# Performance work log

Hardware: AMD Instinct MI355X
Metric: run time of the kernel (lower is better)

## Reference

```python
import jax, jax.numpy as jnp
import numpy as np

NL, NS, NE = 16, 256, 100   # nlatent, nspatial, n_embd
B, P, T = 2, 2, 12


def _xavier(key, shape):
    # torch xavier_uniform: fan_in = shape[1]*prod(rest), fan_out = shape[0]*prod(rest)
    rf = int(np.prod(shape[2:])) if len(shape) > 2 else 1
    fan_in, fan_out = shape[1] * rf, shape[0] * rf
    b = float(np.sqrt(6.0 / (fan_in + fan_out)))
    return jax.random.uniform(key, shape, jnp.float32, -b, b)


def setup_inputs() -> dict:
    key = jax.random.key(0)
    ks = jax.random.split(key, 8)
    x = jax.random.normal(ks[0], (B, P, T, NL, NS), jnp.float32)
    K = _xavier(ks[1], (NS, NS, NL))
    Q = _xavier(ks[2], (NS, NS, NL))
    V = _xavier(ks[3], (NS, NS, NL))
    Aoo = jnp.ones((NS, NS), jnp.float32)
    # Ann is initialized to zeros in the module; use nonzero values so the
    # clamped geometric recurrence over time is actually exercised.
    Ann = jax.random.uniform(ks[4], (NE,), jnp.float32, -0.9, 0.9)
    Aon = _xavier(ks[5], (NS, NS, NE))
    Ano = _xavier(ks[6], (NS, NS, NE))
    w = jnp.ones((NS,), jnp.float32) / NS
    return {"x": x, "K": K, "Q": Q, "V": V, "Aoo": Aoo,
            "Ann": Ann, "Aon": Aon, "Ano": Ano, "w": w}


def reference(x, K, Q, V, Aoo, Ann, Aon, Ano, w):
    # kvt[B,p,T,X,Y] = sum_{x,c} Q[Y,x,c] K[X,x,c] x[B,p,T,c,x]
    kvt = jnp.einsum('Yxc,Xxc,BpTcx->BpTXY', Q, K, x)
    Aon_c = jnp.clip(Aon, -1.0, 1.0)
    Ano_c = jnp.clip(Ano, -1.0, 1.0)

    # t = T-1 term (elementwise Aoo) and t = T-2 term
    h = Aoo[None, None, None] * kvt[:, :, -1:]
    h = h + jnp.einsum('xyn,XYn,BpTXY->BpTxy', Aon_c, Ano_c, kvt[:, :, -2:-1])

    nT = x.shape[2]
    # Ann sequence used in the loop: A_2 = Ann (raw), A_{j+1} = clip(A_j * Ann)
    def step(a, _):
        return jnp.clip(a * Ann, -1.0, 1.0), a
    _, A_seq = jax.lax.scan(step, Ann, None, length=nT - 2)  # [T-2, n], A_seq[j-2]=A_j

    # loop index j=2..T-1 touches time slice t = T-1-j, i.e. t = T-3 .. 0
    s = jnp.einsum('XYn,BpJXY->BpJn', Ano_c, kvt[:, :, :nT - 2])  # J = t in 0..T-3
    A_t = A_seq[::-1]                       # align A_j with time index t = T-1-j
    s2 = jnp.einsum('Jn,BpJn->Bpn', A_t, s)
    h = h + jnp.einsum('xyn,Bpn->Bpxy', Aon_c, s2)[:, :, None]  # [B,p,1,x,y]

    q = jnp.einsum('Xxc,Bpcx->BpcX', V, x[:, :, -1])
    y = jnp.einsum('x,BpcX,BpTXx->BpTc', w, q, h)  # [B,p,1,c]
    return y
```

## Files before the change

### kernel.cpp

```cpp
#include <hip/hip_runtime.h>
#include <hip/hip_fp16.h>


using f32x4 = __attribute__((ext_vector_type(4))) float;
using half8 = __attribute__((ext_vector_type(8))) _Float16;
using half4 = __attribute__((ext_vector_type(4))) _Float16;

#define KVT_STRIDE 3145728ull
#define KS 4

__device__ inline float clip1(float v) { return fminf(fmaxf(v, -1.f), 1.f); }

__device__ inline half8 mul8(uint4 a, uint4 b) {
    half8 x = __builtin_bit_cast(half8, a);
    half8 y = __builtin_bit_cast(half8, b);
    return x * y;
}

__device__ __forceinline__ void gl_lds16(const void* g, void* l) {
    __builtin_amdgcn_global_load_lds(
        (const __attribute__((address_space(1))) void*)g,
        (__attribute__((address_space(3))) void*)l, 16, 0, 0);
}

__global__ void prep_kernel(const float* __restrict__ K, const float* __restrict__ Q,
                            const float* __restrict__ xin,
                            __half* __restrict__ Kh, __half* __restrict__ Qh,
                            __half* __restrict__ u_t)
{
    int b = blockIdx.x, t = threadIdx.x;
    if (b < 512) {
        bool isK = (b < 256);
        int bb = isK ? b : b - 256;
        size_t base = (size_t)bb * 4096 + t * 16;
        const f32x4* src = (const f32x4*)((isK ? K : Q) + base);
        __half* dst = (isK ? Kh : Qh) + base;
        #pragma unroll
        for (int j = 0; j < 2; ++j) {
            f32x4 v0 = src[j * 2], v1 = src[j * 2 + 1];
            half8 h;
            h[0] = (_Float16)v0.x; h[1] = (_Float16)v0.y;
            h[2] = (_Float16)v0.z; h[3] = (_Float16)v0.w;
            h[4] = (_Float16)v1.x; h[5] = (_Float16)v1.y;
            h[6] = (_Float16)v1.z; h[7] = (_Float16)v1.w;
            *(half8*)(dst + j * 8) = h;
        }
    } else {
        int bt = b - 512;
        const float* src = xin + (size_t)bt * 4096;
        int xx = t;
        half8 lo, hi;
        #pragma unroll
        for (int c = 0; c < 8; ++c)  lo[c] = (_Float16)src[c * 256 + xx];
        #pragma unroll
        for (int c = 0; c < 8; ++c)  hi[c] = (_Float16)src[(c + 8) * 256 + xx];
        half8* dst = (half8*)(u_t + (size_t)bt * 4096 + xx * 16);
        dst[0] = lo; dst[1] = hi;
    }
}

__global__ __launch_bounds__(256, 4) void gemm_kvt(
    const __half* __restrict__ Kh, const __half* __restrict__ Qh,
    const __half* __restrict__ u_t, __half* __restrict__ kvtp)
{
    __shared__ __half As[2][128][32];
    __shared__ __half Bs[2][128][32];
    __shared__ __half u_s[1024];

    int bid = blockIdx.x;
    int work = (bid & 7) * 96 + (bid >> 3);
    int kc = work / 192;
    int rem = work - kc * 192;
    int tile = rem / 48;
    int bt = rem - tile * 48;
    int Xb = (tile >> 1) * 128, Yb = (tile & 1) * 128;
    int kbase = kc * 1024;

    int tid = threadIdx.x;
    if (tid < 128)
        *(uint4*)&u_s[tid * 8] = *(const uint4*)(u_t + (size_t)bt * 4096 + kbase + tid * 8);
    __syncthreads();

    int wave = tid >> 6, lane = tid & 63;

    int arow = tid >> 1;
    int apair = (tid & 1) * 2;
    const __half* gA = Kh + (size_t)(Xb + arow) * 4096 + kbase + apair * 8;
    int aswz = (arow >> 1) & 3;
    int asb0 = ((apair + 0) ^ aswz) << 4;
    int asb1 = ((apair + 1) ^ aswz) << 4;

    int srow = lane >> 2;
    int sk = ((lane & 3) ^ ((srow >> 1) & 3)) << 3;
    const __half* gB = Qh + (size_t)(Yb + wave * 16 + srow) * 4096 + kbase + sk;

    int wr = (wave >> 1) * 64, wc = (wave & 1) * 64;
    int lrow = lane & 15, kg = lane >> 4;
    int fb = (kg * 16) ^ (((lrow >> 1) & 3) << 4);

    f32x4 acc[4][4];
    f32x4 zero = {0.f, 0.f, 0.f, 0.f};
    #pragma unroll
    for (int m = 0; m < 4; ++m)
        #pragma unroll
        for (int n = 0; n < 4; ++n) acc[m][n] = zero;

    #define ISSUE_B(s, buf)                                                    \
        do {                                                                   \
            _Pragma("unroll")                                                  \
            for (int i_ = 0; i_ < 2; ++i_)                                     \
                gl_lds16(gB + (size_t)(i_ * 64) * 4096 + (s) * 32,             \
                         &Bs[buf][i_ * 64 + wave * 16][0]);                    \
        } while (0)

    #define WRITE_A(s, r0, r1, buf)                                            \
        do {                                                                   \
            uint4 uv0 = *(const uint4*)&u_s[(s) * 32 + apair * 8];             \
            uint4 uv1 = *(const uint4*)&u_s[(s) * 32 + apair * 8 + 8];         \
            *(half8*)((char*)&As[buf][arow][0] + asb0) = mul8(r0, uv0);        \
            *(half8*)((char*)&As[buf][arow][0] + asb1) = mul8(r1, uv1);        \
        } while (0)

    #define COMPUTE(cur)                                                       \
        do {                                                                   \
            half8 af[4], bf[4];                                                \
            _Pragma("unroll")                                                  \
            for (int m = 0; m < 4; ++m)                                        \
                af[m] = *(const half8*)((const char*)&As[cur][wr + m * 16 + lrow][0] + fb); \
            _Pragma("unroll")                                                  \
            for (int n = 0; n < 4; ++n)                                        \
                bf[n] = *(const half8*)((const char*)&Bs[cur][wc + n * 16 + lrow][0] + fb); \
            _Pragma("unroll")                                                  \
            for (int m = 0; m < 4; ++m)                                        \
                _Pragma("unroll")                                              \
                for (int n = 0; n < 4; ++n)                                    \
                    acc[m][n] = __builtin_amdgcn_mfma_f32_16x16x32_f16(af[m], bf[n], acc[m][n], 0, 0, 0); \
        } while (0)

    #define STEP(s, c0, c1, i0, i1, cur)                                       \
        do {                                                                   \
            if ((s) < 31) asm volatile("s_waitcnt vmcnt(4) lgkmcnt(0)" ::: "memory"); \
            else          asm volatile("s_waitcnt vmcnt(0) lgkmcnt(0)" ::: "memory"); \
            __builtin_amdgcn_s_barrier();                                      \
            __builtin_amdgcn_sched_barrier(0);                                 \
            COMPUTE(cur);                                                      \
            asm volatile("s_waitcnt lgkmcnt(0)" ::: "memory");                 \
            __builtin_amdgcn_s_barrier();                                      \
            __builtin_amdgcn_sched_barrier(0);                                 \
            if ((s) + 2 < 32) {                                                \
                const __half* a_ = gA + ((s) + 2) * 32;                        \
                i0 = *(const uint4*)a_;                                        \
                i1 = *(const uint4*)(a_ + 8);                                  \
                ISSUE_B((s) + 2, cur);                                         \
            }                                                                  \
            if ((s) + 1 < 32) WRITE_A((s) + 1, c0, c1, (cur) ^ 1);             \
        } while (0)

    uint4 aP0, aP1, aC0, aC1;
    aP0 = *(const uint4*)gA;
    aP1 = *(const uint4*)(gA + 8);
    ISSUE_B(0, 0);
    aC0 = *(const uint4*)(gA + 32);
    aC1 = *(const uint4*)(gA + 40);
    ISSUE_B(1, 1);
    WRITE_A(0, aP0, aP1, 0);

    #pragma unroll
    for (int s = 0; s < 32; s += 2) {
        STEP(s,     aC0, aC1, aP0, aP1, 0);
        STEP(s + 1, aP0, aP1, aC0, aC1, 1);
    }
    #undef STEP
    #undef COMPUTE
    #undef WRITE_A
    #undef ISSUE_B

    __half* outp = kvtp + (size_t)kc * KVT_STRIDE + (size_t)bt * 65536;
    int row0 = Xb + wr + kg * 4;
    int col0 = Yb + wc + lrow;
    #pragma unroll
    for (int m = 0; m < 4; ++m)
        #pragma unroll
        for (int n = 0; n < 4; ++n)
            #pragma unroll
            for (int rr = 0; rr < 4; ++rr)
                outp[(size_t)(row0 + m * 16 + rr) * 256 + col0 + n * 16] =
                    __float2half(acc[m][n][rr]);
}

__global__ __launch_bounds__(256) void mid_kernel(
    const float* __restrict__ Ano, const __half* __restrict__ kvtp,
    const float* __restrict__ V, const float* __restrict__ xin,
    const float* __restrict__ Aon, const float* __restrict__ wv,
    float* __restrict__ Sp, float* __restrict__ R, float* __restrict__ W2p)
{
    __shared__ __align__(16) char smem[49792];
    int b = blockIdx.x, tid = threadIdx.x;

    if (b < 256) {
        __half* anoA = (__half*)smem;
        __half* anoB = (__half*)(smem + 12928);
        float (*kvtA)[68] = (float(*)[68])(smem + 25856);
        float (*kvtB)[68] = (float(*)[68])(smem + 37824);
        int k0 = b * 256;

        int lane = tid & 63;
        int bp = tid >> 6;
        bool has2 = lane < 36;
        float acc0[11], acc1[11];
        #pragma unroll
        for (int J = 0; J < 11; ++J) { acc0[J] = 0.f; acc1[J] = 0.f; }

        f32x4 ar[7];
        half8 kr[2][4];

        #define LOAD_SP(cc)                                                    \
            do {                                                               \
                int k0s = k0 + (cc) * 64;                                      \
                const f32x4* asrc = (const f32x4*)(Ano + (size_t)k0s * 100);   \
                _Pragma("unroll")                                              \
                for (int it = 0; it < 7; ++it) {                               \
                    int i = tid + it * 256;                                    \
                    if (i < 1600) ar[it] = __builtin_nontemporal_load(asrc + i); \
                }                                                              \
                _Pragma("unroll")                                              \
                for (int it = 0; it < 2; ++it) {                               \
                    int idx = tid + it * 256;                                  \
                    if (idx < 352) {                                           \
                        int rI = idx >> 3, g = idx & 7;                        \
                        int bpr = rI / 11, Jr = rI - bpr * 11;                 \
                        const __half* p = kvtp + (size_t)(bpr * 12 + Jr) * 65536 + k0s + g * 8; \
                        kr[it][0] = *(const half8*)(p);                        \
                        kr[it][1] = *(const half8*)(p + KVT_STRIDE);           \
                        kr[it][2] = *(const half8*)(p + 2 * KVT_STRIDE);       \
                        kr[it][3] = *(const half8*)(p + 3 * KVT_STRIDE);       \
                    }                                                          \
                }                                                              \
            } while (0)

        #define WRITE_SP(anoDst, kvtDst)                                       \
            do {                                                               \
                _Pragma("unroll")                                              \
                for (int it = 0; it < 7; ++it) {                               \
                    int i = tid + it * 256;                                    \
                    if (i < 1600) {                                            \
                        half4 h;                                               \
                        h[0] = (_Float16)clip1(ar[it].x);                      \
                        h[1] = (_Float16)clip1(ar[it].y);                      \
                        h[2] = (_Float16)clip1(ar[it].z);                      \
                        h[3] = (_Float16)clip1(ar[it].w);                      \
                        *(half4*)&anoDst[i * 4] = h;                           \
                    }                                                          \
                }                                                              \
                _Pragma("unroll")                                              \
                for (int it = 0; it < 2; ++it) {                               \
                    int idx = tid + it * 256;                                  \
                    if (idx < 352) {                                           \
                        int rI = idx >> 3, g = idx & 7;                        \
                        f32x4 lo, hi;                                          \
                        _Pragma("unroll")                                      \
                        for (int j = 0; j < 4; ++j) {                          \
                            lo[j] = (float)kr[it][0][j] + (float)kr[it][1][j]  \
                                  + (float)kr[it][2][j] + (float)kr[it][3][j]; \
                            hi[j] = (float)kr[it][0][j+4] + (float)kr[it][1][j+4] \
                                  + (float)kr[it][2][j+4] + (float)kr[it][3][j+4]; \
                        }                                                      \
                        *(f32x4*)&kvtDst[rI][g * 8]     = lo;                  \
                        *(f32x4*)&kvtDst[rI][g * 8 + 4] = hi;                  \
                    }                                                          \
                }                                                              \
            } while (0)

        #define COMPUTE_SP(anoSrc, kvtSrc)                                     \
            do {                                                               \
                for (int k = 0; k < 64; k += 4) {                              \
                    f32x4 kv[11];                                              \
                    _Pragma("unroll")                                          \
                    for (int J = 0; J < 11; ++J)                               \
                        kv[J] = *(const f32x4*)&kvtSrc[bp * 11 + J][k];        \
                    _Pragma("unroll")                                          \
                    for (int kk = 0; kk < 4; ++kk) {                           \
                        float a0 = (float)anoSrc[(k + kk) * 100 + lane];       \
                        float a1r = (float)anoSrc[(k + kk) * 100 + 64 + lane]; \
                        float a1 = has2 ? a1r : 0.f;                           \
                        _Pragma("unroll")                                      \
                        for (int J = 0; J < 11; ++J) {                         \
                            acc0[J] += kv[J][kk] * a0;                         \
                            acc1[J] += kv[J][kk] * a1;                         \
                        }                                                      \
                    }                                                          \
                }                                                              \
            } while (0)

        LOAD_SP(0);
        WRITE_SP(anoA, kvtA);
        __syncthreads();
        LOAD_SP(1);
        COMPUTE_SP(anoA, kvtA);
        WRITE_SP(anoB, kvtB);
        __syncthreads();
        LOAD_SP(2);
        COMPUTE_SP(anoB, kvtB);
        WRITE_SP(anoA, kvtA);
        __syncthreads();
        LOAD_SP(3);
        COMPUTE_SP(anoA, kvtA);
        WRITE_SP(anoB, kvtB);
        __syncthreads();
        COMPUTE_SP(anoB, kvtB);

        #undef LOAD_SP
        #undef WRITE_SP
        #undef COMPUTE_SP

        float* outb = Sp + ((size_t)b * 4 + bp) * 1100;
        #pragma unroll
        for (int J = 0; J < 11; ++J) {
            outb[J * 100 + lane] = acc0[J];
            if (has2) outb[J * 100 + 64 + lane] = acc1[J];
        }
    } else if (b < 512) {
        float* vrow = (float*)smem;
        int X = b - 256;
        {
            const float4* src = (const float4*)(V + (size_t)X * 4096);
            float4* dst = (float4*)vrow;
            for (int i = tid; i < 1024; i += 256) dst[i] = src[i];
        }
        __syncthreads();
        int bp = tid >> 6, c = (tid >> 2) & 15, g = tid & 3;
        const float* xl = xin + ((size_t)(bp * 12) + 11) * 4096 + c * 256;
        float p = 0.f;
        #pragma unroll 4
        for (int x = g * 64; x < g * 64 + 64; ++x)
            p += xl[x] * vrow[x * 16 + c];
        p += __shfl_xor(p, 1);
        p += __shfl_xor(p, 2);
        if (g == 0) R[((size_t)bp * 256 + X) * 16 + c] = p;
    } else {
        int idx = b - 512;
        int X = idx >> 1, h = idx & 1;
        int g = h * 2 + (tid >> 7), n = tid & 127;
        if (n < 100) {
            const float* base = Aon + (size_t)X * 25600 + (size_t)g * 6400 + n;
            float acc = 0.f;
            for (int bb = 0; bb < 64; ++bb)
                acc += wv[g * 64 + bb] * clip1(__builtin_nontemporal_load(base + (size_t)bb * 100));
            W2p[((size_t)g * 256 + X) * 100 + n] = acc;
        }
    }
}

__global__ void reduce_s(const float* __restrict__ Sp, float* __restrict__ Sq,
                         float* __restrict__ out)
{
    int bid = blockIdx.x;
    int t = threadIdx.x;
    if (bid == 0 && t < 64) out[t] = 0.f;
    int qq = bid & 7, idx = bid >> 3;
    int bp = idx / 11, J = idx - bp * 11;
    if (t >= 100) return;
    float acc = 0.f;
    for (int c = qq * 32; c < qq * 32 + 32; ++c)
        acc += Sp[((size_t)c * 4 + bp) * 1100 + J * 100 + t];
    Sq[(size_t)(qq * 44 + idx) * 100 + t] = acc;
}

__global__ __launch_bounds__(256) void hw_kernel(const float* __restrict__ Aoo,
                                                 const float* __restrict__ wv,
                                                 const __half* __restrict__ kvtp,
                                                 const float* __restrict__ W2p,
                                                 const float* __restrict__ Sq,
                                                 const float* __restrict__ Ann,
                                                 const float* __restrict__ R,
                                                 float* __restrict__ out)
{
    __shared__ float yp[4][16];
    __shared__ float c2s[128];
    int bp = blockIdx.x >> 6, Xg = blockIdx.x & 63;
    int tid = threadIdx.x;

    if (tid < 128) {
        int n = tid;
        float r = 0.f;
        if (n < 100) {
            float S[11];
            #pragma unroll
            for (int J = 0; J < 11; ++J) {
                float s = 0.f;
                #pragma unroll
                for (int qq = 0; qq < 8; ++qq)
                    s += Sq[(size_t)(qq * 44 + bp * 11 + J) * 100 + n];
                S[J] = s;
            }
            float a = Ann[n];
            float seq[10];
            float v = a;
            seq[0] = v;
            #pragma unroll
            for (int s2 = 1; s2 < 10; ++s2) { v = clip1(v * a); seq[s2] = v; }
            r = S[10];
            #pragma unroll
            for (int J = 0; J < 10; ++J)
                r += seq[9 - J] * S[J];
        }
        c2s[n] = r;
    }
    __syncthreads();

    int wave = tid >> 6, lane = tid & 63;
    int X = Xg * 4 + wave;
    size_t base = (size_t)(bp * 12 + 11) * 65536 + (size_t)X * 256;
    const float* ao = Aoo + (size_t)X * 256;
    float red = 0.f;
    #pragma unroll
    for (int qq = 0; qq < 4; ++qq) {
        int xx = qq * 64 + lane;
        float kvv = 0.f;
        #pragma unroll
        for (int c = 0; c < KS; ++c)
            kvv += __half2float(kvtp[(size_t)c * KVT_STRIDE + base + xx]);
        red += wv[xx] * ao[xx] * kvv;
    }
    float w2a = 0.f, w2b = 0.f;
    #pragma unroll
    for (int g = 0; g < 4; ++g) {
        w2a += W2p[((size_t)g * 256 + X) * 100 + lane];
        if (lane < 36) w2b += W2p[((size_t)g * 256 + X) * 100 + 64 + lane];
    }
    red += c2s[lane] * w2a;
    if (lane < 36)
        red += c2s[64 + lane] * w2b;
    #pragma unroll
    for (int off = 32; off; off >>= 1) red += __shfl_xor(red, off);
    if (lane < 16) yp[wave][lane] = red * R[((size_t)bp * 256 + X) * 16 + lane];
    __syncthreads();
    if (tid < 16) {
        float s = yp[0][tid] + yp[1][tid] + yp[2][tid] + yp[3][tid];
        atomicAdd(&out[bp * 16 + tid], s);
    }
}

extern "C" void kernel_launch(void* const* d_in, const int* in_sizes, int n_in,
                              void* d_out, int out_size, void* d_ws, size_t ws_size,
                              hipStream_t stream)
{
    const float* x   = (const float*)d_in[0];
    const float* K   = (const float*)d_in[1];
    const float* Q   = (const float*)d_in[2];
    const float* V   = (const float*)d_in[3];
    const float* Aoo = (const float*)d_in[4];
    const float* Ann = (const float*)d_in[5];
    const float* Aon = (const float*)d_in[6];
    const float* Ano = (const float*)d_in[7];
    const float* wv  = (const float*)d_in[8];
    float* out = (float*)d_out;

    char* ws = (char*)d_ws;
    const size_t o_Qh   = 0;
    const size_t o_Kh   = o_Qh + (size_t)2 * 1024 * 1024;
    const size_t o_ut   = o_Kh + (size_t)2 * 1024 * 1024;
    const size_t o_kvtp = o_ut + (size_t)512 * 1024;
    const size_t o_Sp   = o_kvtp + (size_t)KS * KVT_STRIDE * 2;
    const size_t o_Sq   = o_Sp + (size_t)256 * 4400 * 4;
    const size_t o_W2   = o_Sq + (size_t)35200 * 4 + 64;
    const size_t o_R    = o_W2 + (size_t)102400 * 4;

    __half* Qh  = (__half*)(ws + o_Qh);
    __half* Kh  = (__half*)(ws + o_Kh);
    __half* u_t = (__half*)(ws + o_ut);
    __half* kvtp = (__half*)(ws + o_kvtp);
    float* Sp   = (float*)(ws + o_Sp);
    float* Sq   = (float*)(ws + o_Sq);
    float* W2p  = (float*)(ws + o_W2);
    float* R    = (float*)(ws + o_R);

    hipLaunchKernelGGL(prep_kernel, dim3(560),  dim3(256), 0, stream,
                       K, Q, x, Kh, Qh, u_t);
    hipLaunchKernelGGL(gemm_kvt,    dim3(768),  dim3(256), 0, stream,
                       Kh, Qh, u_t, kvtp);
    hipLaunchKernelGGL(mid_kernel,  dim3(1024), dim3(256), 0, stream,
                       Ano, kvtp, V, x, Aon, wv, Sp, R, W2p);
    hipLaunchKernelGGL(reduce_s,    dim3(352),  dim3(128), 0, stream, Sp, Sq, out);
    hipLaunchKernelGGL(hw_kernel,   dim3(256),  dim3(256), 0, stream,
                       Aoo, wv, kvtp, W2p, Sq, Ann, R, out);
}
```

Baseline: 88.95 us.

## Double K-tile depth in kvt GEMM and single-buffer the A tile

```diff
diff --git a/kernel.cpp b/kernel.cpp
--- a/kernel.cpp
+++ b/kernel.cpp
@@ -59,12 +59,12 @@
     }
 }
 
-__global__ __launch_bounds__(256, 4) void gemm_kvt(
+__global__ __launch_bounds__(256, 3) void gemm_kvt(
     const __half* __restrict__ Kh, const __half* __restrict__ Qh,
     const __half* __restrict__ u_t, __half* __restrict__ kvtp)
 {
-    __shared__ __half As[2][128][32];
-    __shared__ __half Bs[2][128][32];
+    __shared__ __half As[128][64];
+    __shared__ __half Bs[2][128][64];
     __shared__ __half u_s[1024];
 
     int bid = blockIdx.x;
@@ -84,19 +84,18 @@
     int wave = tid >> 6, lane = tid & 63;
 
     int arow = tid >> 1;
-    int apair = (tid & 1) * 2;
-    const __half* gA = Kh + (size_t)(Xb + arow) * 4096 + kbase + apair * 8;
-    int aswz = (arow >> 1) & 3;
-    int asb0 = ((apair + 0) ^ aswz) << 4;
-    int asb1 = ((apair + 1) ^ aswz) << 4;
-
-    int srow = lane >> 2;
-    int sk = ((lane & 3) ^ ((srow >> 1) & 3)) << 3;
-    const __half* gB = Qh + (size_t)(Yb + wave * 16 + srow) * 4096 + kbase + sk;
+    int ap0 = (tid & 1) * 4;
+    const __half* gA = Kh + (size_t)(Xb + arow) * 4096 + kbase + ap0 * 8;
+    int arsw = arow & 7;
+
+    int brow = wave * 32 + (lane >> 3);
+    int bq = (lane & 7) ^ ((lane >> 3) & 7);
+    const __half* gB = Qh + (size_t)(Yb + brow) * 4096 + kbase + bq * 8;
 
     int wr = (wave >> 1) * 64, wc = (wave & 1) * 64;
     int lrow = lane & 15, kg = lane >> 4;
-    int fb = (kg * 16) ^ (((lrow >> 1) & 3) << 4);
+    int fb0 = ((0 * 4 + kg) ^ (lrow & 7)) << 4;
+    int fb1 = ((1 * 4 + kg) ^ (lrow & 7)) << 4;
 
     f32x4 acc[4][4];
     f32x4 zero = {0.f, 0.f, 0.f, 0.f};
@@ -104,42 +103,57 @@
     for (int m = 0; m < 4; ++m)
         #pragma unroll
         for (int n = 0; n < 4; ++n) acc[m][n] = zero;
+
+    #define LOAD_A(s, rg)                                                      \
+        do {                                                                   \
+            const __half* a_ = gA + (s) * 64;                                  \
+            _Pragma("unroll")                                                  \
+            for (int j_ = 0; j_ < 4; ++j_)                                     \
+                rg[j_] = *(const uint4*)(a_ + j_ * 8);                         \
+        } while (0)
 
     #define ISSUE_B(s, buf)                                                    \
         do {                                                                   \
             _Pragma("unroll")                                                  \
-            for (int i_ = 0; i_ < 2; ++i_)                                     \
-                gl_lds16(gB + (size_t)(i_ * 64) * 4096 + (s) * 32,             \
-                         &Bs[buf][i_ * 64 + wave * 16][0]);                    \
+            for (int i_ = 0; i_ < 4; ++i_)                                     \
+                gl_lds16(gB + (size_t)(i_ * 8) * 4096 + (s) * 64,              \
+                         &Bs[buf][wave * 32 + i_ * 8][0]);                     \
         } while (0)
 
-    #define WRITE_A(s, r0, r1, buf)                                            \
+    #define WRITE_A(s, rg)                                                     \
         do {                                                                   \
-            uint4 uv0 = *(const uint4*)&u_s[(s) * 32 + apair * 8];             \
-            uint4 uv1 = *(const uint4*)&u_s[(s) * 32 + apair * 8 + 8];         \
-            *(half8*)((char*)&As[buf][arow][0] + asb0) = mul8(r0, uv0);        \
-            *(half8*)((char*)&As[buf][arow][0] + asb1) = mul8(r1, uv1);        \
+            _Pragma("unroll")                                                  \
+            for (int j_ = 0; j_ < 4; ++j_) {                                   \
+                int p_ = ap0 + j_;                                             \
+                uint4 uv_ = *(const uint4*)&u_s[(s) * 64 + p_ * 8];            \
+                *(half8*)((char*)&As[arow][0] + ((p_ ^ arsw) << 4)) =          \
+                    mul8(rg[j_], uv_);                                         \
+            }                                                                  \
         } while (0)
 
     #define COMPUTE(cur)                                                       \
         do {                                                                   \
-            half8 af[4], bf[4];                                                \
             _Pragma("unroll")                                                  \
-            for (int m = 0; m < 4; ++m)                                        \
-                af[m] = *(const half8*)((const char*)&As[cur][wr + m * 16 + lrow][0] + fb); \
-            _Pragma("unroll")                                                  \
-            for (int n = 0; n < 4; ++n)                                        \
-                bf[n] = *(const half8*)((const char*)&Bs[cur][wc + n * 16 + lrow][0] + fb); \
-            _Pragma("unroll")                                                  \
-            for (int m = 0; m < 4; ++m)                                        \
+            for (int kh = 0; kh < 2; ++kh) {                                   \
+                int fbk = kh ? fb1 : fb0;                                      \
+                half8 af[4], bf[4];                                            \
+                _Pragma("unroll")                                              \
+                for (int m = 0; m < 4; ++m)                                    \
+                    af[m] = *(const half8*)((const char*)&As[wr + m * 16 + lrow][0] + fbk); \
                 _Pragma("unroll")                                              \
                 for (int n = 0; n < 4; ++n)                                    \
-                    acc[m][n] = __builtin_amdgcn_mfma_f32_16x16x32_f16(af[m], bf[n], acc[m][n], 0, 0, 0); \
+                    bf[n] = *(const half8*)((const char*)&Bs[cur][wc + n * 16 + lrow][0] + fbk); \
+                _Pragma("unroll")                                              \
+                for (int m = 0; m < 4; ++m)                                    \
+                    _Pragma("unroll")                                          \
+                    for (int n = 0; n < 4; ++n)                                \
+                        acc[m][n] = __builtin_amdgcn_mfma_f32_16x16x32_f16(af[m], bf[n], acc[m][n], 0, 0, 0); \
+            }                                                                  \
         } while (0)
 
-    #define STEP(s, c0, c1, i0, i1, cur)                                       \
+    #define STEP(s, cset, iset, cur)                                           \
         do {                                                                   \
-            if ((s) < 31) asm volatile("s_waitcnt vmcnt(4) lgkmcnt(0)" ::: "memory"); \
+            if ((s) < 15) asm volatile("s_waitcnt vmcnt(8) lgkmcnt(0)" ::: "memory"); \
             else          asm volatile("s_waitcnt vmcnt(0) lgkmcnt(0)" ::: "memory"); \
             __builtin_amdgcn_s_barrier();                                      \
             __builtin_amdgcn_sched_barrier(0);                                 \
@@ -147,33 +161,30 @@
             asm volatile("s_waitcnt lgkmcnt(0)" ::: "memory");                 \
             __builtin_amdgcn_s_barrier();                                      \
             __builtin_amdgcn_sched_barrier(0);                                 \
-            if ((s) + 2 < 32) {                                                \
-                const __half* a_ = gA + ((s) + 2) * 32;                        \
-                i0 = *(const uint4*)a_;                                        \
-                i1 = *(const uint4*)(a_ + 8);                                  \
+            if ((s) + 2 < 16) {                                                \
+                LOAD_A((s) + 2, iset);                                         \
                 ISSUE_B((s) + 2, cur);                                         \
             }                                                                  \
-            if ((s) + 1 < 32) WRITE_A((s) + 1, c0, c1, (cur) ^ 1);             \
+            if ((s) + 1 < 16) WRITE_A((s) + 1, cset);                          \
         } while (0)
 
-    uint4 aP0, aP1, aC0, aC1;
-    aP0 = *(const uint4*)gA;
-    aP1 = *(const uint4*)(gA + 8);
+    uint4 aP[4], aC[4];
+    LOAD_A(0, aP);
     ISSUE_B(0, 0);
-    aC0 = *(const uint4*)(gA + 32);
-    aC1 = *(const uint4*)(gA + 40);
+    LOAD_A(1, aC);
     ISSUE_B(1, 1);
-    WRITE_A(0, aP0, aP1, 0);
-
-    #pragma unroll
-    for (int s = 0; s < 32; s += 2) {
-        STEP(s,     aC0, aC1, aP0, aP1, 0);
-        STEP(s + 1, aP0, aP1, aC0, aC1, 1);
+    WRITE_A(0, aP);
+
+    #pragma unroll
+    for (int s = 0; s < 16; s += 2) {
+        STEP(s,     aC, aP, 0);
+        STEP(s + 1, aP, aC, 1);
     }
     #undef STEP
     #undef COMPUTE
     #undef WRITE_A
     #undef ISSUE_B
+    #undef LOAD_A
 
     __half* outp = kvtp + (size_t)kc * KVT_STRIDE + (size_t)bt * 65536;
     int row0 = Xb + wr + kg * 4;
```

Result: no change. 87.86 us (-1.2%).
